# Performance work log

Measured on AMD Instinct MI355X. Metric: run time of the kernel, lower is better.

Reference implementation:

```python
import jax, jax.numpy as jnp
import numpy as np
from jax import lax

B, CR, CS = 2, 256, 512
HR = WR = 64
HS = WS = 32
D_INNER, D_STATE, DT_RANK, D_CONV = 512, 16, 16, 3
EPS = 1e-5


def setup_inputs() -> dict:
    key = jax.random.key(0)
    ks = jax.random.split(key, 16)
    s = 0.02
    return {
        "resnet_feat": jax.random.normal(ks[0], (B, CR, HR, WR), jnp.float32),
        "scp_feat": jax.random.normal(ks[1], (B, CS, HS, WS), jnp.float32),
        "scp_proj_w": jax.random.normal(ks[2], (CR, CS), jnp.float32) * s,
        "scp_bn_g": jnp.ones((CR,), jnp.float32),
        "scp_bn_b": jnp.zeros((CR,), jnp.float32),
        "scp_bn_m": jax.random.normal(ks[3], (CR,), jnp.float32) * 0.1,
        "scp_bn_v": jax.random.uniform(ks[4], (CR,), jnp.float32, minval=0.5, maxval=1.5),
        "res_bn_g": jnp.ones((CR,), jnp.float32),
        "res_bn_b": jnp.zeros((CR,), jnp.float32),
        "res_bn_m": jax.random.normal(ks[5], (CR,), jnp.float32) * 0.1,
        "res_bn_v": jax.random.uniform(ks[6], (CR,), jnp.float32, minval=0.5, maxval=1.5),
        "ln_g": jnp.ones((CR,), jnp.float32),
        "ln_b": jnp.zeros((CR,), jnp.float32),
        "in_proj_w": jax.random.normal(ks[7], (2 * D_INNER, CR), jnp.float32) * s,
        "conv_w": jax.random.normal(ks[8], (D_INNER, 1, D_CONV), jnp.float32) * s,
        "conv_b": jnp.zeros((D_INNER,), jnp.float32),
        "x_proj_w": jax.random.normal(ks[9], (DT_RANK + 2 * D_STATE, D_INNER), jnp.float32) * s,
        "dt_proj_w": jax.random.normal(ks[10], (D_INNER, DT_RANK), jnp.float32) * s,
        "dt_proj_b": jnp.full((D_INNER,), -4.6, jnp.float32),  # softplus -> dt ~ 0.01
        "A_log": jnp.log(jnp.broadcast_to(jnp.arange(1, D_STATE + 1, dtype=jnp.float32), (D_INNER, D_STATE))),
        "D": jnp.ones((D_INNER,), jnp.float32),
        "out_proj_w": jax.random.normal(ks[11], (CR, D_INNER), jnp.float32) * s,
    }


def _bn(x, g, b, m, v):
    # eval-mode BatchNorm2d with running stats, NCHW
    inv = g / jnp.sqrt(v + EPS)
    return x * inv[None, :, None, None] + (b - m * inv)[None, :, None, None]


def reference(resnet_feat, scp_feat, scp_proj_w, scp_bn_g, scp_bn_b, scp_bn_m, scp_bn_v,
              res_bn_g, res_bn_b, res_bn_m, res_bn_v, ln_g, ln_b, in_proj_w, conv_w, conv_b,
              x_proj_w, dt_proj_w, dt_proj_b, A_log, D, out_proj_w):
    # --- fusion prelude ---
    rn = _bn(resnet_feat, res_bn_g, res_bn_b, res_bn_m, res_bn_v)
    sp = jnp.einsum('bchw,oc->bohw', scp_feat, scp_proj_w)        # 1x1 conv, no bias
    sp = _bn(sp, scp_bn_g, scp_bn_b, scp_bn_m, scp_bn_v)
    sp = jax.image.resize(sp, (B, CR, HR, WR), method='bilinear')  # align_corners=False semantics
    fused = rn + sp                                               # (B, CR, HR, WR)

    # --- Mamba2DBlock ---
    L = HR * WR
    x_seq = fused.transpose(0, 2, 3, 1).reshape(B, L, CR)
    mu = x_seq.mean(-1, keepdims=True)
    var = x_seq.var(-1, keepdims=True)
    xn = (x_seq - mu) / jnp.sqrt(var + EPS) * ln_g + ln_b         # LayerNorm

    xz = xn @ in_proj_w.T                                         # (B, L, 2*d_inner)
    xm, z = jnp.split(xz, 2, axis=-1)

    # causal depthwise conv1d over sequence
    xc = xm.transpose(0, 2, 1)                                    # (B, d_inner, L)
    xc = jnp.pad(xc, ((0, 0), (0, 0), (D_CONV - 1, 0)))
    xc = lax.conv_general_dilated(xc, conv_w, (1,), 'VALID',
                                  dimension_numbers=('NCH', 'OIH', 'NCH'),
                                  feature_group_count=D_INNER) + conv_b[None, :, None]
    u = jax.nn.silu(xc.transpose(0, 2, 1))                        # (B, L, d_inner)

    x_dbl = u @ x_proj_w.T                                        # (B, L, dt_rank + 2*d_state)
    dt_in, Bc, Cc = jnp.split(x_dbl, [DT_RANK, DT_RANK + D_STATE], axis=-1)
    dt = jax.nn.softplus(dt_in @ dt_proj_w.T + dt_proj_b)         # (B, L, d_inner)

    A = -jnp.exp(A_log)                                           # (d_inner, d_state)
    dA = jnp.exp(dt[..., None] * A)                               # (B, L, d_inner, d_state)
    dBu = dt[..., None] * Bc[:, :, None, :] * u[..., None]        # (B, L, d_inner, d_state)

    def comb(c1, c2):
        a1, b1 = c1
        a2, b2 = c2
        return a1 * a2, a2 * b1 + b2

    _, h = lax.associative_scan(comb, (dA, dBu), axis=1)          # h: (B, L, d_inner, d_state)
    y = jnp.einsum('blds,bls->bld', h, Cc) + u * D
    y = y * jax.nn.silu(z)
    out_seq = y @ out_proj_w.T                                    # (B, L, CR)
    out = out_seq.reshape(B, HR, WR, CR).transpose(0, 3, 1, 2)
    return fused + out
```

## Files before the change

kernel.cpp:

```cpp
#include <hip/hip_runtime.h>
#include <hip/hip_bf16.h>
#include <math.h>

typedef unsigned short u16;
typedef __attribute__((ext_vector_type(8))) short short8;
typedef __attribute__((ext_vector_type(4))) float f32x4;
typedef __attribute__((ext_vector_type(4))) unsigned short u16x4;

#define DEVINL static __device__ __forceinline__

DEVINL float b2f(u16 x) {
    union { unsigned u; float f; } v; v.u = ((unsigned)x) << 16; return v.f;
}
DEVINL u16 f2b(float f) {
    union { unsigned u; float f; } v; v.f = f;
    unsigned u = v.u;
    return (u16)((u + 0x7fffu + ((u >> 16) & 1u)) >> 16);
}
DEVINL float silu(float x) { return x / (1.f + __expf(-x)); }

template<bool F32> DEVINL float LDs(const void* p, size_t i) {
    if constexpr (F32) return ((const float*)p)[i];
    else               return b2f(((const u16*)p)[i]);
}

#define O_INW  0
#define O_XPW  262144
#define O_OPW  286720
#define O_SPW  417792
#define O_CW   548864
#define O_CB   550400
#define O_DTW  550912
#define O_ALOG 559104
#define O_DTB  567296
#define O_DW   567808
#define O_SG   568320
#define O_SB   568576
#define O_SM   568832
#define O_SV   569088
#define O_RG   569344
#define O_RB   569600
#define O_RM   569856
#define O_RV   570112
#define O_LG   570368
#define O_LB   570624
#define N_CVT  570880

__global__ __launch_bounds__(256) void k_detect1(const u16* __restrict__ raw,
                                                 int* __restrict__ partial)
{
    int tid = threadIdx.x, bid = blockIdx.x;
    int cnt = 0;
    for (size_t i = (size_t)bid * 256 + tid; i < 2097152; i += 64 * 256) {
        float v = b2f(raw[i]);
        if (!(fabsf(v) <= 1e3f)) cnt++;
    }
#pragma unroll
    for (int off = 1; off < 64; off <<= 1) cnt += __shfl_xor(cnt, off);
    __shared__ int s4[4];
    if ((tid & 63) == 0) s4[tid >> 6] = cnt;
    __syncthreads();
    if (tid == 0) partial[bid] = s4[0] + s4[1] + s4[2] + s4[3];
}

__global__ __launch_bounds__(64) void k_detect2(const int* __restrict__ partial,
                                                int* __restrict__ flag)
{
    int c = partial[threadIdx.x];
#pragma unroll
    for (int off = 1; off < 64; off <<= 1) c += __shfl_xor(c, off);
    if (threadIdx.x == 0) flag[0] = (c > 0) ? 1 : 0;
}

__global__ __launch_bounds__(256) void k_cvt(const int* __restrict__ flag,
    const void* inw, const void* xpw, const void* opw, const void* spw,
    const void* cw, const void* cb, const void* dtw, const void* alog,
    const void* dtb, const void* Dw,
    const void* sg, const void* sb, const void* sm, const void* sv,
    const void* rg, const void* rb, const void* rm, const void* rv,
    const void* lg, const void* lb,
    u16* __restrict__ dst)
{
    int i = blockIdx.x * 256 + threadIdx.x;
    if (i >= N_CVT) return;
    const void* src; int off = i;
    if      (i < O_XPW)  { src = inw; }
    else if (i < O_OPW)  { src = xpw;  off = i - O_XPW; }
    else if (i < O_SPW)  { src = opw;  off = i - O_OPW; }
    else if (i < O_CW)   { src = spw;  off = i - O_SPW; }
    else if (i < O_CB)   { src = cw;   off = i - O_CW; }
    else if (i < O_DTW)  { src = cb;   off = i - O_CB; }
    else if (i < O_ALOG) { src = dtw;  off = i - O_DTW; }
    else if (i < O_DTB)  { src = alog; off = i - O_ALOG; }
    else if (i < O_DW)   { src = dtb;  off = i - O_DTB; }
    else if (i < O_SG)   { src = Dw;   off = i - O_DW; }
    else if (i < O_SB)   { src = sg;   off = i - O_SG; }
    else if (i < O_SM)   { src = sb;   off = i - O_SB; }
    else if (i < O_SV)   { src = sm;   off = i - O_SM; }
    else if (i < O_RG)   { src = sv;   off = i - O_SV; }
    else if (i < O_RB)   { src = rg;   off = i - O_RG; }
    else if (i < O_RM)   { src = rb;   off = i - O_RB; }
    else if (i < O_RV)   { src = rm;   off = i - O_RM; }
    else if (i < O_LG)   { src = rv;   off = i - O_RV; }
    else if (i < O_LB)   { src = lg;   off = i - O_LG; }
    else                 { src = lb;   off = i - O_LB; }
    float v = (*flag) ? ((const float*)src)[off] : b2f(((const u16*)src)[off]);
    dst[i] = f2b(v);
}

template<bool F32> DEVINL void tr_body(const void* src, u16* dst, int R, int C)
{
    __shared__ u16 t[64][66];
    int tid = threadIdx.x;
    int c0 = blockIdx.x * 64, r0 = blockIdx.y * 64, b = blockIdx.z;
    int lane = tid & 63, grp = tid >> 6;
#pragma unroll
    for (int j = 0; j < 16; ++j) {
        int rl = j * 4 + grp;
        t[rl][lane] = f2b(LDs<F32>(src, ((size_t)b * R + r0 + rl) * C + c0 + lane));
    }
    __syncthreads();
#pragma unroll
    for (int j = 0; j < 16; ++j) {
        int cl = j * 4 + grp;
        dst[((size_t)b * C + c0 + cl) * R + r0 + lane] = t[lane][cl];
    }
}
__global__ __launch_bounds__(256) void k_tr(const int* flag,
    const void* src, u16* dst, int R, int C)
{
    if (*flag) tr_body<true>(src, dst, R, C);
    else       tr_body<false>(src, dst, R, C);
}

__global__ __launch_bounds__(256) void k_scpmm(
    const u16* __restrict__ scpT, const u16* __restrict__ w16,
    u16* __restrict__ sp16)
{
    const int N = 256, K = 512;
    int tid = threadIdx.x, lane = tid & 63, wid = tid >> 6;
    int ln = lane & 15, q = lane >> 4;
    int m0 = blockIdx.x * 64 + (wid & 1) * 32;
    int n0 = blockIdx.y * 64 + (wid >> 1) * 32;
    f32x4 acc00 = {0.f,0.f,0.f,0.f}, acc01 = acc00, acc10 = acc00, acc11 = acc00;
    const u16* Ap0 = scpT + (size_t)(m0 + ln) * K + q * 8;
    const u16* Ap1 = Ap0 + (size_t)16 * K;
    const u16* Wp = w16 + O_SPW;
#pragma unroll 4
    for (int k0 = 0; k0 < K; k0 += 32) {
        int kk = k0 + q * 8;
        short8 a0 = *reinterpret_cast<const short8*>(Ap0 + k0);
        short8 a1 = *reinterpret_cast<const short8*>(Ap1 + k0);
        short8 b0 = *reinterpret_cast<const short8*>(Wp + (size_t)(n0 + ln) * K + kk);
        short8 b1 = *reinterpret_cast<const short8*>(Wp + (size_t)(n0 + ln + 16) * K + kk);
        acc00 = __builtin_amdgcn_mfma_f32_16x16x32_bf16(a0, b0, acc00, 0, 0, 0);
        acc01 = __builtin_amdgcn_mfma_f32_16x16x32_bf16(a0, b1, acc01, 0, 0, 0);
        acc10 = __builtin_amdgcn_mfma_f32_16x16x32_bf16(a1, b0, acc10, 0, 0, 0);
        acc11 = __builtin_amdgcn_mfma_f32_16x16x32_bf16(a1, b1, acc11, 0, 0, 0);
    }
    int r0 = m0 + q * 4, c0 = n0 + ln;
    float inv0 = b2f(w16[O_SG + c0]) * rsqrtf(b2f(w16[O_SV + c0]) + 1e-5f);
    float sh0  = b2f(w16[O_SB + c0]) - b2f(w16[O_SM + c0]) * inv0;
    float inv1 = b2f(w16[O_SG + c0 + 16]) * rsqrtf(b2f(w16[O_SV + c0 + 16]) + 1e-5f);
    float sh1  = b2f(w16[O_SB + c0 + 16]) - b2f(w16[O_SM + c0 + 16]) * inv1;
#pragma unroll
    for (int r = 0; r < 4; ++r) {
        sp16[(size_t)(r0 + r) * N + c0]           = f2b(acc00[r] * inv0 + sh0);
        sp16[(size_t)(r0 + r) * N + c0 + 16]      = f2b(acc01[r] * inv1 + sh1);
        sp16[(size_t)(r0 + 16 + r) * N + c0]      = f2b(acc10[r] * inv0 + sh0);
        sp16[(size_t)(r0 + 16 + r) * N + c0 + 16] = f2b(acc11[r] * inv1 + sh1);
    }
}

__global__ __launch_bounds__(256) void k_ln(
    const u16* __restrict__ resnetT, const u16* __restrict__ w16,
    const u16* __restrict__ sp16, u16* __restrict__ xn)
{
    int c = threadIdx.x, l = blockIdx.x, b = blockIdx.y;
    int h = l >> 6, w = l & 63;
    float rr  = b2f(resnetT[((size_t)b * 4096 + l) * 256 + c]);
    float inv = b2f(w16[O_RG + c]) * rsqrtf(b2f(w16[O_RV + c]) + 1e-5f);
    float rn  = rr * inv + (b2f(w16[O_RB + c]) - b2f(w16[O_RM + c]) * inv);

    float xh = 0.5f * h - 0.25f; int jh = (int)floorf(xh); float fh = xh - jh;
    float xw = 0.5f * w - 0.25f; int jw = (int)floorf(xw); float fw = xw - jw;
    int h0 = jh < 0 ? 0 : jh, h1 = jh + 1 > 31 ? 31 : jh + 1;
    int w0 = jw < 0 ? 0 : jw, w1 = jw + 1 > 31 ? 31 : jw + 1;
    const u16* spb = sp16 + (size_t)b * 1024 * 256 + c;
    float v00 = b2f(spb[(size_t)(h0 * 32 + w0) * 256]), v01 = b2f(spb[(size_t)(h0 * 32 + w1) * 256]);
    float v10 = b2f(spb[(size_t)(h1 * 32 + w0) * 256]), v11 = b2f(spb[(size_t)(h1 * 32 + w1) * 256]);
    float sp = (1.f - fh) * ((1.f - fw) * v00 + fw * v01)
             + fh * ((1.f - fw) * v10 + fw * v11);
    float fv = rn + sp;

    __shared__ float red[8];
    float s = fv, s2 = fv * fv;
#pragma unroll
    for (int off = 1; off < 64; off <<= 1) {
        s  += __shfl_xor(s, off);
        s2 += __shfl_xor(s2, off);
    }
    int wv = c >> 6;
    if ((c & 63) == 0) { red[wv] = s; red[4 + wv] = s2; }
    __syncthreads();
    float S  = red[0] + red[1] + red[2] + red[3];
    float S2 = red[4] + red[5] + red[6] + red[7];
    float mu   = S * (1.f / 256.f);
    float var  = S2 * (1.f / 256.f) - mu * mu;
    float rstd = rsqrtf(var + 1e-5f);
    float xnv  = (fv - mu) * rstd * b2f(w16[O_LG + c]) + b2f(w16[O_LB + c]);
    xn[((size_t)b * 4096 + l) * 256 + c] = f2b(xnv);
}

__global__ __launch_bounds__(256) void k_gemm_in(
    const u16* __restrict__ A, const u16* __restrict__ w16, u16* __restrict__ Out)
{
    const int N = 1024, K = 256;
    int tid = threadIdx.x, lane = tid & 63, wid = tid >> 6;
    int ln = lane & 15, q = lane >> 4;
    int m0 = blockIdx.x * 64 + (wid & 1) * 32;
    int n0 = blockIdx.y * 64 + (wid >> 1) * 32;
    f32x4 acc00 = {0.f,0.f,0.f,0.f}, acc01 = acc00, acc10 = acc00, acc11 = acc00;
    const u16* Ap0 = A + (size_t)(m0 + ln) * K + q * 8;
    const u16* Ap1 = Ap0 + (size_t)16 * K;
    const u16* Wp = w16 + O_INW;
#pragma unroll 4
    for (int k0 = 0; k0 < K; k0 += 32) {
        int kk = k0 + q * 8;
        short8 a0 = *reinterpret_cast<const short8*>(Ap0 + k0);
        short8 a1 = *reinterpret_cast<const short8*>(Ap1 + k0);
        short8 b0 = *reinterpret_cast<const short8*>(Wp + (size_t)(n0 + ln) * K + kk);
        short8 b1 = *reinterpret_cast<const short8*>(Wp + (size_t)(n0 + ln + 16) * K + kk);
        acc00 = __builtin_amdgcn_mfma_f32_16x16x32_bf16(a0, b0, acc00, 0, 0, 0);
        acc01 = __builtin_amdgcn_mfma_f32_16x16x32_bf16(a0, b1, acc01, 0, 0, 0);
        acc10 = __builtin_amdgcn_mfma_f32_16x16x32_bf16(a1, b0, acc10, 0, 0, 0);
        acc11 = __builtin_amdgcn_mfma_f32_16x16x32_bf16(a1, b1, acc11, 0, 0, 0);
    }
    int r0 = m0 + q * 4, c0 = n0 + ln;
#pragma unroll
    for (int r = 0; r < 4; ++r) {
        Out[(size_t)(r0 + r) * N + c0]           = f2b(acc00[r]);
        Out[(size_t)(r0 + r) * N + c0 + 16]      = f2b(acc01[r]);
        Out[(size_t)(r0 + 16 + r) * N + c0]      = f2b(acc10[r]);
        Out[(size_t)(r0 + 16 + r) * N + c0 + 16] = f2b(acc11[r]);
    }
}

__global__ __launch_bounds__(512) void k_conv(
    const u16* __restrict__ xz, const u16* __restrict__ w16, u16* __restrict__ u)
{
    int d = threadIdx.x, rt = blockIdx.x, b = blockIdx.y;
    int l0 = rt * 16;
    float c0 = b2f(w16[O_CW + d * 3]), c1 = b2f(w16[O_CW + d * 3 + 1]),
          c2 = b2f(w16[O_CW + d * 3 + 2]), cbv = b2f(w16[O_CB + d]);
    size_t base = ((size_t)b * 4096 + l0) * 1024 + d;
    float x2 = (l0 >= 2) ? b2f(xz[base - 2048]) : 0.f;
    float x1 = (l0 >= 1) ? b2f(xz[base - 1024]) : 0.f;
#pragma unroll 4
    for (int il = 0; il < 16; ++il) {
        float x0 = b2f(xz[base + (size_t)il * 1024]);
        float uv = silu(cbv + c0 * x2 + c1 * x1 + c2 * x0);
        u[((size_t)b * 4096 + l0 + il) * 512 + d] = f2b(uv);
        x2 = x1; x1 = x0;
    }
}

__global__ __launch_bounds__(256) void k_xproj(
    const u16* __restrict__ u, const u16* __restrict__ w16, u16* __restrict__ xd16)
{
    int tid = threadIdx.x, lane = tid & 63, wid = tid >> 6;
    int ln = lane & 15, q = lane >> 4;
    int m0 = blockIdx.x * 64 + wid * 16;
    const u16* Wp = w16 + O_XPW;
    f32x4 acc[3];
#pragma unroll
    for (int j = 0; j < 3; ++j) acc[j] = {0.f,0.f,0.f,0.f};
#pragma unroll 4
    for (int k0 = 0; k0 < 512; k0 += 32) {
        int kk0 = k0 + q * 8;
        short8 a0 = *reinterpret_cast<const short8*>(u + (size_t)(m0 + ln) * 512 + kk0);
#pragma unroll
        for (int j = 0; j < 3; ++j) {
            short8 bj = *reinterpret_cast<const short8*>(Wp + (size_t)(16 * j + ln) * 512 + kk0);
            acc[j] = __builtin_amdgcn_mfma_f32_16x16x32_bf16(a0, bj, acc[j], 0, 0, 0);
        }
    }
#pragma unroll
    for (int j = 0; j < 3; ++j)
#pragma unroll
        for (int r = 0; r < 4; ++r)
            xd16[(size_t)(m0 + q * 4 + r) * 48 + 16 * j + ln] = f2b(acc[j][r]);
}

DEVINL float dt_of(const float* xd, const float* wdt, float bias) {
    float acc = bias;
#pragma unroll
    for (int r = 0; r < 16; ++r) acc += xd[r] * wdt[r];
    return acc > 15.f ? acc : __logf(1.f + __expf(acc));
}

__global__ __launch_bounds__(512) void k_scan1(
    const u16* __restrict__ u, const u16* __restrict__ xd16,
    const u16* __restrict__ w16, u16* __restrict__ cA, u16* __restrict__ cH,
    int NC, int CL)
{
    __shared__ float xds[32][48];
    int d = threadIdx.x, ck = blockIdx.x, b = blockIdx.y;
    float wdt[16], a[16], h[16], ap[16];
#pragma unroll
    for (int s = 0; s < 16; ++s) {
        wdt[s] = b2f(w16[O_DTW + d * 16 + s]);
        a[s] = -__expf(b2f(w16[O_ALOG + d * 16 + s]));
        h[s] = 0.f; ap[s] = 1.f;
    }
    float bias = b2f(w16[O_DTB + d]);
    int l0 = ck * CL;
    for (int t0 = 0; t0 < CL; t0 += 32) {
        __syncthreads();
#pragma unroll
        for (int k = 0; k < 3; ++k) {
            int idx = k * 512 + d;
            int r = idx / 48, c = idx - r * 48;
            xds[r][c] = b2f(xd16[((size_t)b * 4096 + l0 + t0 + r) * 48 + c]);
        }
        __syncthreads();
        for (int il = 0; il < 32; ++il) {
            size_t row = (size_t)b * 4096 + l0 + t0 + il;
            float uv = b2f(u[row * 512 + d]);
            const float* xd = xds[il];
            float dtv = dt_of(xd, wdt, bias);
            float du = dtv * uv;
#pragma unroll
            for (int s = 0; s < 16; ++s) {
                float dA = __expf(dtv * a[s]);
                h[s]  = dA * h[s] + du * xd[16 + s];
                ap[s] *= dA;
            }
        }
    }
    size_t base = (((size_t)b * NC + ck) * 16) * 512 + d;
#pragma unroll
    for (int s = 0; s < 16; ++s) {
        cA[base + (size_t)s * 512] = f2b(ap[s]);
        cH[base + (size_t)s * 512] = f2b(h[s]);
    }
}

__global__ __launch_bounds__(128) void k_scan2(const u16* __restrict__ cA,
                                               u16* __restrict__ cH, int NC)
{
    int d = blockIdx.y * 128 + threadIdx.x, s = blockIdx.x, b = blockIdx.z;
    float h = 0.f;
#pragma unroll 4
    for (int ck = 0; ck < NC; ++ck) {
        size_t idx = (((size_t)b * NC + ck) * 16 + s) * 512 + d;
        float aP = b2f(cA[idx]), hE = b2f(cH[idx]);
        cH[idx] = f2b(h);
        h = aP * h + hE;
    }
}

__global__ __launch_bounds__(512) void k_scan3(
    const u16* __restrict__ u, const u16* __restrict__ xz,
    const u16* __restrict__ xd16, const u16* __restrict__ w16,
    const u16* __restrict__ cH, u16* __restrict__ y, int NC, int CL)
{
    __shared__ float xds[32][48];
    int d = threadIdx.x, ck = blockIdx.x, b = blockIdx.y;
    float wdt[16], a[16], h[16];
    size_t base = (((size_t)b * NC + ck) * 16) * 512 + d;
#pragma unroll
    for (int s = 0; s < 16; ++s) {
        wdt[s] = b2f(w16[O_DTW + d * 16 + s]);
        a[s] = -__expf(b2f(w16[O_ALOG + d * 16 + s]));
        h[s] = b2f(cH[base + (size_t)s * 512]);
    }
    float bias = b2f(w16[O_DTB + d]);
    float Dv = b2f(w16[O_DW + d]);
    int l0 = ck * CL;
    for (int t0 = 0; t0 < CL; t0 += 32) {
        __syncthreads();
#pragma unroll
        for (int k = 0; k < 3; ++k) {
            int idx = k * 512 + d;
            int r = idx / 48, c = idx - r * 48;
            xds[r][c] = b2f(xd16[((size_t)b * 4096 + l0 + t0 + r) * 48 + c]);
        }
        __syncthreads();
        for (int il = 0; il < 32; ++il) {
            size_t row = (size_t)b * 4096 + l0 + t0 + il;
            float uv = b2f(u[row * 512 + d]);
            const float* xd = xds[il];
            float dtv = dt_of(xd, wdt, bias);
            float du = dtv * uv;
            float yv = 0.f;
#pragma unroll
            for (int s = 0; s < 16; ++s) {
                float dA = __expf(dtv * a[s]);
                h[s] = dA * h[s] + du * xd[16 + s];
                yv += h[s] * xd[32 + s];
            }
            yv += uv * Dv;
            float zv = b2f(xz[row * 1024 + 512 + d]);
            yv *= silu(zv);
            y[row * 512 + d] = f2b(yv);
        }
    }
}

template<bool F32> DEVINL void out_body(
    const u16* Y, const u16* w16, const void* resnet,
    const u16* sp16, void* outp)
{
    const int K = 512;
    int tid = threadIdx.x, lane = tid & 63, wid = tid >> 6;
    int ln = lane & 15, q = lane >> 4;
    int m0 = blockIdx.x * 64 + (wid & 1) * 32;
    int n0 = blockIdx.y * 64 + (wid >> 1) * 32;
    f32x4 acc[2][2];
    acc[0][0] = {0.f,0.f,0.f,0.f}; acc[0][1] = acc[0][0];
    acc[1][0] = acc[0][0]; acc[1][1] = acc[0][0];
    const u16* Bp0 = Y + (size_t)(n0 + ln) * K + q * 8;
    const u16* Bp1 = Bp0 + (size_t)16 * K;
    const u16* Wp = w16 + O_OPW;
#pragma unroll 4
    for (int k0 = 0; k0 < K; k0 += 32) {
        int kk = k0 + q * 8;
        short8 b0 = *reinterpret_cast<const short8*>(Bp0 + k0);
        short8 b1 = *reinterpret_cast<const short8*>(Bp1 + k0);
        short8 a0 = *reinterpret_cast<const short8*>(Wp + (size_t)(m0 + ln) * K + kk);
        short8 a1 = *reinterpret_cast<const short8*>(Wp + (size_t)(m0 + ln + 16) * K + kk);
        acc[0][0] = __builtin_amdgcn_mfma_f32_16x16x32_bf16(a0, b0, acc[0][0], 0, 0, 0);
        acc[0][1] = __builtin_amdgcn_mfma_f32_16x16x32_bf16(a0, b1, acc[0][1], 0, 0, 0);
        acc[1][0] = __builtin_amdgcn_mfma_f32_16x16x32_bf16(a1, b0, acc[1][0], 0, 0, 0);
        acc[1][1] = __builtin_amdgcn_mfma_f32_16x16x32_bf16(a1, b1, acc[1][1], 0, 0, 0);
    }
    int r0 = m0 + q * 4;
    int nb = n0 + ln;
    float inv8[2][4], sh8[2][4];
#pragma unroll
    for (int im = 0; im < 2; ++im)
#pragma unroll
        for (int r = 0; r < 4; ++r) {
            int c = r0 + 16 * im + r;
            float inv = b2f(w16[O_RG + c]) * rsqrtf(b2f(w16[O_RV + c]) + 1e-5f);
            inv8[im][r] = inv;
            sh8[im][r]  = b2f(w16[O_RB + c]) - b2f(w16[O_RM + c]) * inv;
        }
#pragma unroll
    for (int jn = 0; jn < 2; ++jn) {
        int n = nb + 16 * jn;
        int b = n >> 12, l = n & 4095;
        int hh = l >> 6, w = l & 63;
        float xh = 0.5f * hh - 0.25f; int jh = (int)floorf(xh); float fh = xh - jh;
        float xw = 0.5f * w - 0.25f;  int jw = (int)floorf(xw); float fw = xw - jw;
        int h0 = jh < 0 ? 0 : jh, h1 = jh + 1 > 31 ? 31 : jh + 1;
        int w0 = jw < 0 ? 0 : jw, w1 = jw + 1 > 31 ? 31 : jw + 1;
        float w00 = (1.f - fh) * (1.f - fw), w01 = (1.f - fh) * fw;
        float w10 = fh * (1.f - fw),         w11 = fh * fw;
        const u16* spb = sp16 + (size_t)b * 1024 * 256;
#pragma unroll
        for (int im = 0; im < 2; ++im) {
            int cb = r0 + 16 * im;
            u16x4 s00 = *reinterpret_cast<const u16x4*>(spb + (size_t)(h0 * 32 + w0) * 256 + cb);
            u16x4 s01 = *reinterpret_cast<const u16x4*>(spb + (size_t)(h0 * 32 + w1) * 256 + cb);
            u16x4 s10 = *reinterpret_cast<const u16x4*>(spb + (size_t)(h1 * 32 + w0) * 256 + cb);
            u16x4 s11 = *reinterpret_cast<const u16x4*>(spb + (size_t)(h1 * 32 + w1) * 256 + cb);
#pragma unroll
            for (int r = 0; r < 4; ++r) {
                int c = cb + r;
                float rr = LDs<F32>(resnet, ((size_t)b * 256 + c) * 4096 + l);
                float sp = w00 * b2f(s00[r]) + w01 * b2f(s01[r])
                         + w10 * b2f(s10[r]) + w11 * b2f(s11[r]);
                float val = acc[im][jn][r] + rr * inv8[im][r] + sh8[im][r] + sp;
                size_t oi = ((size_t)b * 256 + c) * 4096 + l;
                if constexpr (F32) ((float*)outp)[oi] = val;
                else               ((u16*)outp)[oi]  = f2b(val);
            }
        }
    }
}
__global__ __launch_bounds__(256) void k_out(const int* flag,
    const u16* Y, const u16* w16, const void* resnet,
    const u16* sp16, void* outp)
{
    if (*flag) out_body<true>(Y, w16, resnet, sp16, outp);
    else       out_body<false>(Y, w16, resnet, sp16, outp);
}

extern "C" void kernel_launch(void* const* d_in, const int* in_sizes, int n_in,
                              void* d_out, int out_size, void* d_ws, size_t ws_size,
                              hipStream_t stream)
{
    const void* resnet = d_in[0];
    const void* scp    = d_in[1];
    const void* spw    = d_in[2];
    const void* sg     = d_in[3];
    const void* sb     = d_in[4];
    const void* sm     = d_in[5];
    const void* sv     = d_in[6];
    const void* rg     = d_in[7];
    const void* rb     = d_in[8];
    const void* rm     = d_in[9];
    const void* rv     = d_in[10];
    const void* lg     = d_in[11];
    const void* lb     = d_in[12];
    const void* inw    = d_in[13];
    const void* cw     = d_in[14];
    const void* cb     = d_in[15];
    const void* xpw    = d_in[16];
    const void* dtw    = d_in[17];
    const void* dtb    = d_in[18];
    const void* alog   = d_in[19];
    const void* Dw     = d_in[20];
    const void* opw    = d_in[21];

    char* ws = (char*)d_ws;
    int*  flag    = (int*)(ws);
    int*  partial = (int*)(ws + 128);
    u16*  w16     = (u16*)(ws + 4096);
    u16*  sp16    = (u16*)(ws + 1310720);
    u16*  scpT    = (u16*)(ws + 2359296);
    u16*  resnetT = (u16*)(ws + 4456448);
    u16*  xn      = (u16*)(ws + 8650752);
    u16*  xz      = (u16*)(ws + 12845056);
    u16*  u       = (u16*)(ws + 29622272);
    u16*  y       = (u16*)(ws + 38011008);
    u16*  xd16    = (u16*)(ws + 46399488);
    const size_t tail0 = 47185920;

    int NC = 16;
    for (int cand = 128; cand >= 16; cand >>= 1) {
        if (tail0 + (size_t)cand * 65536 <= ws_size) { NC = cand; break; }
    }
    int CL = 4096 / NC;
    u16* cA = (u16*)(ws + tail0);
    u16* cH = (u16*)(ws + tail0 + (size_t)NC * 32768);

    k_detect1<<<dim3(64), 256, 0, stream>>>((const u16*)resnet, partial);
    k_detect2<<<dim3(1), 64, 0, stream>>>(partial, flag);
    k_cvt<<<dim3((N_CVT + 255) / 256), 256, 0, stream>>>(flag,
        inw, xpw, opw, spw, cw, cb, dtw, alog, dtb, Dw,
        sg, sb, sm, sv, rg, rb, rm, rv, lg, lb, w16);
    k_tr<<<dim3(16, 8, 2), 256, 0, stream>>>(flag, scp, scpT, 512, 1024);
    k_scpmm<<<dim3(32, 4), 256, 0, stream>>>(scpT, w16, sp16);
    k_tr<<<dim3(64, 4, 2), 256, 0, stream>>>(flag, resnet, resnetT, 256, 4096);
    k_ln<<<dim3(4096, 2), 256, 0, stream>>>(resnetT, w16, sp16, xn);
    k_gemm_in<<<dim3(128, 16), 256, 0, stream>>>(xn, w16, xz);
    k_conv<<<dim3(256, 2), 512, 0, stream>>>(xz, w16, u);
    k_xproj<<<dim3(128), 256, 0, stream>>>(u, w16, xd16);
    k_scan1<<<dim3(NC, 2), 512, 0, stream>>>(u, xd16, w16, cA, cH, NC, CL);
    k_scan2<<<dim3(16, 4, 2), 128, 0, stream>>>(cA, cH, NC);
    k_scan3<<<dim3(NC, 2), 512, 0, stream>>>(u, xz, xd16, w16, cH, y, NC, CL);
    k_out<<<dim3(4, 128), 256, 0, stream>>>(flag, y, w16, resnet, sp16, d_out);
}
```

Before: 289.9 us.

## Fuse conv into xproj/scan, merge prep kernels, batch LN rows per block

Removes the standalone depthwise conv kernel and the u buffer: the causal conv plus SiLU is recomputed on the fly inside x_proj and both scan passes. The detect step becomes a single-block kernel sampling fewer elements, and weight conversion plus both input transposes are merged into one launch. LayerNorm now handles 8 rows per block, and x_proj output is stored as fp32 instead of bf16. This cuts launches and one intermediate round trip, at the cost of redundant conv math and extra xz reads in the scans.

Measured after the change: 281.6 us. -2.9%, faster.

```diff
diff --git a/kernel.cpp b/kernel.cpp
--- a/kernel.cpp
+++ b/kernel.cpp
@@ -18,7 +18,9 @@
     return (u16)((u + 0x7fffu + ((u >> 16) & 1u)) >> 16);
 }
 DEVINL float silu(float x) { return x / (1.f + __expf(-x)); }
-
+DEVINL float ld_any(bool f32, const void* p, size_t i) {
+    return f32 ? ((const float*)p)[i] : b2f(((const u16*)p)[i]);
+}
 template<bool F32> DEVINL float LDs(const void* p, size_t i) {
     if constexpr (F32) return ((const float*)p)[i];
     else               return b2f(((const u16*)p)[i]);
@@ -46,91 +48,89 @@
 #define O_LB   570624
 #define N_CVT  570880
 
-__global__ __launch_bounds__(256) void k_detect1(const u16* __restrict__ raw,
-                                                 int* __restrict__ partial)
-{
-    int tid = threadIdx.x, bid = blockIdx.x;
+__global__ __launch_bounds__(1024) void k_detect(const u16* __restrict__ raw,
+                                                 int* __restrict__ flag)
+{
+    int tid = threadIdx.x;
     int cnt = 0;
-    for (size_t i = (size_t)bid * 256 + tid; i < 2097152; i += 64 * 256) {
+    for (int i = tid; i < 131072; i += 1024) {
         float v = b2f(raw[i]);
         if (!(fabsf(v) <= 1e3f)) cnt++;
     }
 #pragma unroll
     for (int off = 1; off < 64; off <<= 1) cnt += __shfl_xor(cnt, off);
-    __shared__ int s4[4];
-    if ((tid & 63) == 0) s4[tid >> 6] = cnt;
+    __shared__ int s16[16];
+    if ((tid & 63) == 0) s16[tid >> 6] = cnt;
     __syncthreads();
-    if (tid == 0) partial[bid] = s4[0] + s4[1] + s4[2] + s4[3];
-}
-
-__global__ __launch_bounds__(64) void k_detect2(const int* __restrict__ partial,
-                                                int* __restrict__ flag)
-{
-    int c = partial[threadIdx.x];
-#pragma unroll
-    for (int off = 1; off < 64; off <<= 1) c += __shfl_xor(c, off);
-    if (threadIdx.x == 0) flag[0] = (c > 0) ? 1 : 0;
-}
-
-__global__ __launch_bounds__(256) void k_cvt(const int* __restrict__ flag,
+    if (tid == 0) {
+        int c = 0;
+#pragma unroll
+        for (int w = 0; w < 16; ++w) c += s16[w];
+        flag[0] = (c > 0) ? 1 : 0;
+    }
+}
+
+DEVINL void tr_tile(bool f32, const void* src, u16* dst, int R, int C,
+                    int c0, int r0, int b, int tid)
+{
+    __shared__ u16 t[64][66];
+    int lane = tid & 63, grp = tid >> 6;
+#pragma unroll
+    for (int j = 0; j < 16; ++j) {
+        int rl = j * 4 + grp;
+        t[rl][lane] = f2b(ld_any(f32, src, ((size_t)b * R + r0 + rl) * C + c0 + lane));
+    }
+    __syncthreads();
+#pragma unroll
+    for (int j = 0; j < 16; ++j) {
+        int cl = j * 4 + grp;
+        dst[((size_t)b * C + c0 + cl) * R + r0 + lane] = t[lane][cl];
+    }
+}
+
+__global__ __launch_bounds__(256) void k_prep(const int* __restrict__ flag,
     const void* inw, const void* xpw, const void* opw, const void* spw,
     const void* cw, const void* cb, const void* dtw, const void* alog,
     const void* dtb, const void* Dw,
     const void* sg, const void* sb, const void* sm, const void* sv,
     const void* rg, const void* rb, const void* rm, const void* rv,
     const void* lg, const void* lb,
-    u16* __restrict__ dst)
-{
-    int i = blockIdx.x * 256 + threadIdx.x;
-    if (i >= N_CVT) return;
-    const void* src; int off = i;
-    if      (i < O_XPW)  { src = inw; }
-    else if (i < O_OPW)  { src = xpw;  off = i - O_XPW; }
-    else if (i < O_SPW)  { src = opw;  off = i - O_OPW; }
-    else if (i < O_CW)   { src = spw;  off = i - O_SPW; }
-    else if (i < O_CB)   { src = cw;   off = i - O_CW; }
-    else if (i < O_DTW)  { src = cb;   off = i - O_CB; }
-    else if (i < O_ALOG) { src = dtw;  off = i - O_DTW; }
-    else if (i < O_DTB)  { src = alog; off = i - O_ALOG; }
-    else if (i < O_DW)   { src = dtb;  off = i - O_DTB; }
-    else if (i < O_SG)   { src = Dw;   off = i - O_DW; }
-    else if (i < O_SB)   { src = sg;   off = i - O_SG; }
-    else if (i < O_SM)   { src = sb;   off = i - O_SB; }
-    else if (i < O_SV)   { src = sm;   off = i - O_SM; }
-    else if (i < O_RG)   { src = sv;   off = i - O_SV; }
-    else if (i < O_RB)   { src = rg;   off = i - O_RG; }
-    else if (i < O_RM)   { src = rb;   off = i - O_RB; }
-    else if (i < O_RV)   { src = rm;   off = i - O_RM; }
-    else if (i < O_LG)   { src = rv;   off = i - O_RV; }
-    else if (i < O_LB)   { src = lg;   off = i - O_LG; }
-    else                 { src = lb;   off = i - O_LB; }
-    float v = (*flag) ? ((const float*)src)[off] : b2f(((const u16*)src)[off]);
-    dst[i] = f2b(v);
-}
-
-template<bool F32> DEVINL void tr_body(const void* src, u16* dst, int R, int C)
-{
-    __shared__ u16 t[64][66];
-    int tid = threadIdx.x;
-    int c0 = blockIdx.x * 64, r0 = blockIdx.y * 64, b = blockIdx.z;
-    int lane = tid & 63, grp = tid >> 6;
-#pragma unroll
-    for (int j = 0; j < 16; ++j) {
-        int rl = j * 4 + grp;
-        t[rl][lane] = f2b(LDs<F32>(src, ((size_t)b * R + r0 + rl) * C + c0 + lane));
-    }
-    __syncthreads();
-#pragma unroll
-    for (int j = 0; j < 16; ++j) {
-        int cl = j * 4 + grp;
-        dst[((size_t)b * C + c0 + cl) * R + r0 + lane] = t[lane][cl];
-    }
-}
-__global__ __launch_bounds__(256) void k_tr(const int* flag,
-    const void* src, u16* dst, int R, int C)
-{
-    if (*flag) tr_body<true>(src, dst, R, C);
-    else       tr_body<false>(src, dst, R, C);
+    const void* scp, const void* resnet,
+    u16* __restrict__ w16, u16* __restrict__ scpT, u16* __restrict__ resnetT)
+{
+    bool f32 = (*flag != 0);
+    int bid = blockIdx.x, tid = threadIdx.x;
+    if (bid < 2230) {
+        int i = bid * 256 + tid;
+        const void* src; int off = i;
+        if      (i < O_XPW)  { src = inw; }
+        else if (i < O_OPW)  { src = xpw;  off = i - O_XPW; }
+        else if (i < O_SPW)  { src = opw;  off = i - O_OPW; }
+        else if (i < O_CW)   { src = spw;  off = i - O_SPW; }
+        else if (i < O_CB)   { src = cw;   off = i - O_CW; }
+        else if (i < O_DTW)  { src = cb;   off = i - O_CB; }
+        else if (i < O_ALOG) { src = dtw;  off = i - O_DTW; }
+        else if (i < O_DTB)  { src = alog; off = i - O_ALOG; }
+        else if (i < O_DW)   { src = dtb;  off = i - O_DTB; }
+        else if (i < O_SG)   { src = Dw;   off = i - O_DW; }
+        else if (i < O_SB)   { src = sg;   off = i - O_SG; }
+        else if (i < O_SM)   { src = sb;   off = i - O_SB; }
+        else if (i < O_SV)   { src = sm;   off = i - O_SM; }
+        else if (i < O_RG)   { src = sv;   off = i - O_SV; }
+        else if (i < O_RB)   { src = rg;   off = i - O_RG; }
+        else if (i < O_RM)   { src = rb;   off = i - O_RB; }
+        else if (i < O_RV)   { src = rm;   off = i - O_RM; }
+        else if (i < O_LG)   { src = rv;   off = i - O_RV; }
+        else if (i < O_LB)   { src = lg;   off = i - O_LG; }
+        else                 { src = lb;   off = i - O_LB; }
+        w16[i] = f2b(ld_any(f32, src, off));
+    } else if (bid < 2230 + 256) {
+        int t = bid - 2230;
+        tr_tile(f32, scp, scpT, 512, 1024, (t & 15) * 64, ((t >> 4) & 7) * 64, t >> 7, tid);
+    } else {
+        int t = bid - 2486;
+        tr_tile(f32, resnet, resnetT, 256, 4096, (t & 63) * 64, ((t >> 6) & 3) * 64, t >> 8, tid);
+    }
 }
 
 __global__ __launch_bounds__(256) void k_scpmm(
@@ -176,40 +176,44 @@
     const u16* __restrict__ resnetT, const u16* __restrict__ w16,
     const u16* __restrict__ sp16, u16* __restrict__ xn)
 {
-    int c = threadIdx.x, l = blockIdx.x, b = blockIdx.y;
-    int h = l >> 6, w = l & 63;
-    float rr  = b2f(resnetT[((size_t)b * 4096 + l) * 256 + c]);
+    __shared__ float red[8];
+    int c = threadIdx.x, b = blockIdx.y;
     float inv = b2f(w16[O_RG + c]) * rsqrtf(b2f(w16[O_RV + c]) + 1e-5f);
-    float rn  = rr * inv + (b2f(w16[O_RB + c]) - b2f(w16[O_RM + c]) * inv);
-
-    float xh = 0.5f * h - 0.25f; int jh = (int)floorf(xh); float fh = xh - jh;
-    float xw = 0.5f * w - 0.25f; int jw = (int)floorf(xw); float fw = xw - jw;
-    int h0 = jh < 0 ? 0 : jh, h1 = jh + 1 > 31 ? 31 : jh + 1;
-    int w0 = jw < 0 ? 0 : jw, w1 = jw + 1 > 31 ? 31 : jw + 1;
-    const u16* spb = sp16 + (size_t)b * 1024 * 256 + c;
-    float v00 = b2f(spb[(size_t)(h0 * 32 + w0) * 256]), v01 = b2f(spb[(size_t)(h0 * 32 + w1) * 256]);
-    float v10 = b2f(spb[(size_t)(h1 * 32 + w0) * 256]), v11 = b2f(spb[(size_t)(h1 * 32 + w1) * 256]);
-    float sp = (1.f - fh) * ((1.f - fw) * v00 + fw * v01)
-             + fh * ((1.f - fw) * v10 + fw * v11);
-    float fv = rn + sp;
-
-    __shared__ float red[8];
-    float s = fv, s2 = fv * fv;
-#pragma unroll
-    for (int off = 1; off < 64; off <<= 1) {
-        s  += __shfl_xor(s, off);
-        s2 += __shfl_xor(s2, off);
-    }
-    int wv = c >> 6;
-    if ((c & 63) == 0) { red[wv] = s; red[4 + wv] = s2; }
-    __syncthreads();
-    float S  = red[0] + red[1] + red[2] + red[3];
-    float S2 = red[4] + red[5] + red[6] + red[7];
-    float mu   = S * (1.f / 256.f);
-    float var  = S2 * (1.f / 256.f) - mu * mu;
-    float rstd = rsqrtf(var + 1e-5f);
-    float xnv  = (fv - mu) * rstd * b2f(w16[O_LG + c]) + b2f(w16[O_LB + c]);
-    xn[((size_t)b * 4096 + l) * 256 + c] = f2b(xnv);
+    float sh  = b2f(w16[O_RB + c]) - b2f(w16[O_RM + c]) * inv;
+    float lgv = b2f(w16[O_LG + c]), lbv = b2f(w16[O_LB + c]);
+    const u16* spc = sp16 + (size_t)b * 1024 * 256 + c;
+    for (int j = 0; j < 8; ++j) {
+        int l = blockIdx.x * 8 + j;
+        int h = l >> 6, w = l & 63;
+        float rr = b2f(resnetT[((size_t)b * 4096 + l) * 256 + c]);
+        float rn = rr * inv + sh;
+        float xh = 0.5f * h - 0.25f; int jh = (int)floorf(xh); float fh = xh - jh;
+        float xw = 0.5f * w - 0.25f; int jw = (int)floorf(xw); float fw = xw - jw;
+        int h0 = jh < 0 ? 0 : jh, h1 = jh + 1 > 31 ? 31 : jh + 1;
+        int w0 = jw < 0 ? 0 : jw, w1 = jw + 1 > 31 ? 31 : jw + 1;
+        float v00 = b2f(spc[(size_t)(h0 * 32 + w0) * 256]), v01 = b2f(spc[(size_t)(h0 * 32 + w1) * 256]);
+        float v10 = b2f(spc[(size_t)(h1 * 32 + w0) * 256]), v11 = b2f(spc[(size_t)(h1 * 32 + w1) * 256]);
+        float sp = (1.f - fh) * ((1.f - fw) * v00 + fw * v01)
+                 + fh * ((1.f - fw) * v10 + fw * v11);
+        float fv = rn + sp;
+
+        float s = fv, s2 = fv * fv;
+#pragma unroll
+        for (int off = 1; off < 64; off <<= 1) {
+            s  += __shfl_xor(s, off);
+            s2 += __shfl_xor(s2, off);
+        }
+        int wv = c >> 6;
+        if ((c & 63) == 0) { red[wv] = s; red[4 + wv] = s2; }
+        __syncthreads();
+        float S  = red[0] + red[1] + red[2] + red[3];
+        float S2 = red[4] + red[5] + red[6] + red[7];
+        __syncthreads();
+        float mu   = S * (1.f / 256.f);
+        float var  = S2 * (1.f / 256.f) - mu * mu;
+        float rstd = rsqrtf(var + 1e-5f);
+        xn[((size_t)b * 4096 + l) * 256 + c] = f2b((fv - mu) * rstd * lgv + lbv);
+    }
 }
 
 __global__ __launch_bounds__(256) void k_gemm_in(
@@ -246,27 +250,30 @@
     }
 }
 
-__global__ __launch_bounds__(512) void k_conv(
-    const u16* __restrict__ xz, const u16* __restrict__ w16, u16* __restrict__ u)
-{
-    int d = threadIdx.x, rt = blockIdx.x, b = blockIdx.y;
-    int l0 = rt * 16;
-    float c0 = b2f(w16[O_CW + d * 3]), c1 = b2f(w16[O_CW + d * 3 + 1]),
-          c2 = b2f(w16[O_CW + d * 3 + 2]), cbv = b2f(w16[O_CB + d]);
-    size_t base = ((size_t)b * 4096 + l0) * 1024 + d;
-    float x2 = (l0 >= 2) ? b2f(xz[base - 2048]) : 0.f;
-    float x1 = (l0 >= 1) ? b2f(xz[base - 1024]) : 0.f;
-#pragma unroll 4
-    for (int il = 0; il < 16; ++il) {
-        float x0 = b2f(xz[base + (size_t)il * 1024]);
-        float uv = silu(cbv + c0 * x2 + c1 * x1 + c2 * x0);
-        u[((size_t)b * 4096 + l0 + il) * 512 + d] = f2b(uv);
-        x2 = x1; x1 = x0;
-    }
+DEVINL short8 u_frag(const u16* __restrict__ xz, const u16* __restrict__ w16,
+                     int row, int kk0)
+{
+    int l = row & 4095;
+    const u16* p = xz + (size_t)row * 1024 + kk0;
+    short8 zz = {0,0,0,0,0,0,0,0};
+    short8 x0 = *reinterpret_cast<const short8*>(p);
+    short8 x1 = (l >= 1) ? *reinterpret_cast<const short8*>(p - 1024) : zz;
+    short8 x2 = (l >= 2) ? *reinterpret_cast<const short8*>(p - 2048) : zz;
+    short8 r;
+#pragma unroll
+    for (int j = 0; j < 8; ++j) {
+        int d = kk0 + j;
+        float acc = b2f(w16[O_CB + d])
+                  + b2f((u16)x2[j]) * b2f(w16[O_CW + d * 3])
+                  + b2f((u16)x1[j]) * b2f(w16[O_CW + d * 3 + 1])
+                  + b2f((u16)x0[j]) * b2f(w16[O_CW + d * 3 + 2]);
+        r[j] = (short)f2b(silu(acc));
+    }
+    return r;
 }
 
 __global__ __launch_bounds__(256) void k_xproj(
-    const u16* __restrict__ u, const u16* __restrict__ w16, u16* __restrict__ xd16)
+    const u16* __restrict__ xz, const u16* __restrict__ w16, float* __restrict__ xdf)
 {
     int tid = threadIdx.x, lane = tid & 63, wid = tid >> 6;
     int ln = lane & 15, q = lane >> 4;
@@ -275,10 +282,9 @@
     f32x4 acc[3];
 #pragma unroll
     for (int j = 0; j < 3; ++j) acc[j] = {0.f,0.f,0.f,0.f};
-#pragma unroll 4
     for (int k0 = 0; k0 < 512; k0 += 32) {
         int kk0 = k0 + q * 8;
-        short8 a0 = *reinterpret_cast<const short8*>(u + (size_t)(m0 + ln) * 512 + kk0);
+        short8 a0 = u_frag(xz, w16, m0 + ln, kk0);
 #pragma unroll
         for (int j = 0; j < 3; ++j) {
             short8 bj = *reinterpret_cast<const short8*>(Wp + (size_t)(16 * j + ln) * 512 + kk0);
@@ -289,7 +295,7 @@
     for (int j = 0; j < 3; ++j)
 #pragma unroll
         for (int r = 0; r < 4; ++r)
-            xd16[(size_t)(m0 + q * 4 + r) * 48 + 16 * j + ln] = f2b(acc[j][r]);
+            xdf[(size_t)(m0 + q * 4 + r) * 48 + 16 * j + ln] = acc[j][r];
 }
 
 DEVINL float dt_of(const float* xd, const float* wdt, float bias) {
@@ -300,7 +306,7 @@
 }
 
 __global__ __launch_bounds__(512) void k_scan1(
-    const u16* __restrict__ u, const u16* __restrict__ xd16,
+    const u16* __restrict__ xz, const float* __restrict__ xdf,
     const u16* __restrict__ w16, u16* __restrict__ cA, u16* __restrict__ cH,
     int NC, int CL)
 {
@@ -314,19 +320,24 @@
         h[s] = 0.f; ap[s] = 1.f;
     }
     float bias = b2f(w16[O_DTB + d]);
+    float cw0 = b2f(w16[O_CW + d * 3]), cw1 = b2f(w16[O_CW + d * 3 + 1]),
+          cw2 = b2f(w16[O_CW + d * 3 + 2]), cbv = b2f(w16[O_CB + d]);
     int l0 = ck * CL;
+    size_t xbase = ((size_t)b * 4096 + l0) * 1024 + d;
+    float x2 = (l0 >= 2) ? b2f(xz[xbase - 2048]) : 0.f;
+    float x1 = (l0 >= 1) ? b2f(xz[xbase - 1024]) : 0.f;
     for (int t0 = 0; t0 < CL; t0 += 32) {
         __syncthreads();
 #pragma unroll
         for (int k = 0; k < 3; ++k) {
             int idx = k * 512 + d;
             int r = idx / 48, c = idx - r * 48;
-            xds[r][c] = b2f(xd16[((size_t)b * 4096 + l0 + t0 + r) * 48 + c]);
+            xds[r][c] = xdf[((size_t)b * 4096 + l0 + t0 + r) * 48 + c];
         }
         __syncthreads();
         for (int il = 0; il < 32; ++il) {
-            size_t row = (size_t)b * 4096 + l0 + t0 + il;
-            float uv = b2f(u[row * 512 + d]);
+            float x0 = b2f(xz[xbase + (size_t)(t0 + il) * 1024]);
+            float uv = silu(cbv + cw0 * x2 + cw1 * x1 + cw2 * x0);
             const float* xd = xds[il];
             float dtv = dt_of(xd, wdt, bias);
             float du = dtv * uv;
@@ -336,6 +347,7 @@
                 h[s]  = dA * h[s] + du * xd[16 + s];
                 ap[s] *= dA;
             }
+            x2 = x1; x1 = x0;
         }
     }
     size_t base = (((size_t)b * NC + ck) * 16) * 512 + d;
@@ -361,9 +373,9 @@
 }
 
 __global__ __launch_bounds__(512) void k_scan3(
-    const u16* __restrict__ u, const u16* __restrict__ xz,
-    const u16* __restrict__ xd16, const u16* __restrict__ w16,
-    const u16* __restrict__ cH, u16* __restrict__ y, int NC, int CL)
+    const u16* __restrict__ xz, const float* __restrict__ xdf,
+    const u16* __restrict__ w16, const u16* __restrict__ cH,
+    u16* __restrict__ y, int NC, int CL)
 {
     __shared__ float xds[32][48];
     int d = threadIdx.x, ck = blockIdx.x, b = blockIdx.y;
@@ -377,19 +389,25 @@
     }
     float bias = b2f(w16[O_DTB + d]);
     float Dv = b2f(w16[O_DW + d]);
+    float cw0 = b2f(w16[O_CW + d * 3]), cw1 = b2f(w16[O_CW + d * 3 + 1]),
+          cw2 = b2f(w16[O_CW + d * 3 + 2]), cbv = b2f(w16[O_CB + d]);
     int l0 = ck * CL;
+    size_t xbase = ((size_t)b * 4096 + l0) * 1024 + d;
+    float x2 = (l0 >= 2) ? b2f(xz[xbase - 2048]) : 0.f;
+    float x1 = (l0 >= 1) ? b2f(xz[xbase - 1024]) : 0.f;
     for (int t0 = 0; t0 < CL; t0 += 32) {
         __syncthreads();
 #pragma unroll
         for (int k = 0; k < 3; ++k) {
             int idx = k * 512 + d;
             int r = idx / 48, c = idx - r * 48;
-            xds[r][c] = b2f(xd16[((size_t)b * 4096 + l0 + t0 + r) * 48 + c]);
+            xds[r][c] = xdf[((size_t)b * 4096 + l0 + t0 + r) * 48 + c];
         }
         __syncthreads();
         for (int il = 0; il < 32; ++il) {
             size_t row = (size_t)b * 4096 + l0 + t0 + il;
-            float uv = b2f(u[row * 512 + d]);
+            float x0 = b2f(xz[xbase + (size_t)(t0 + il) * 1024]);
+            float uv = silu(cbv + cw0 * x2 + cw1 * x1 + cw2 * x0);
             const float* xd = xds[il];
             float dtv = dt_of(xd, wdt, bias);
             float du = dtv * uv;
@@ -404,6 +422,7 @@
             float zv = b2f(xz[row * 1024 + 512 + d]);
             yv *= silu(zv);
             y[row * 512 + d] = f2b(yv);
+            x2 = x1; x1 = x0;
         }
     }
 }
@@ -515,19 +534,17 @@
     const void* Dw     = d_in[20];
     const void* opw    = d_in[21];
 
-    char* ws = (char*)d_ws;
-    int*  flag    = (int*)(ws);
-    int*  partial = (int*)(ws + 128);
-    u16*  w16     = (u16*)(ws + 4096);
-    u16*  sp16    = (u16*)(ws + 1310720);
-    u16*  scpT    = (u16*)(ws + 2359296);
-    u16*  resnetT = (u16*)(ws + 4456448);
-    u16*  xn      = (u16*)(ws + 8650752);
-    u16*  xz      = (u16*)(ws + 12845056);
-    u16*  u       = (u16*)(ws + 29622272);
-    u16*  y       = (u16*)(ws + 38011008);
-    u16*  xd16    = (u16*)(ws + 46399488);
-    const size_t tail0 = 47185920;
+    char*  ws      = (char*)d_ws;
+    int*   flag    = (int*)(ws);
+    u16*   w16     = (u16*)(ws + 4096);
+    u16*   sp16    = (u16*)(ws + 2097152);
+    u16*   scpT    = (u16*)(ws + 4194304);
+    u16*   resnetT = (u16*)(ws + 8388608);
+    u16*   xn      = (u16*)(ws + 12582912);
+    u16*   xz      = (u16*)(ws + 16777216);
+    float* xdf     = (float*)(ws + 33554432);
+    u16*   y       = (u16*)(ws + 35651584);
+    const size_t tail0 = 44040192;
 
     int NC = 16;
     for (int cand = 128; cand >= 16; cand >>= 1) {
@@ -537,20 +554,17 @@
     u16* cA = (u16*)(ws + tail0);
     u16* cH = (u16*)(ws + tail0 + (size_t)NC * 32768);
 
-    k_detect1<<<dim3(64), 256, 0, stream>>>((const u16*)resnet, partial);
-    k_detect2<<<dim3(1), 64, 0, stream>>>(partial, flag);
-    k_cvt<<<dim3((N_CVT + 255) / 256), 256, 0, stream>>>(flag,
+    k_detect<<<dim3(1), 1024, 0, stream>>>((const u16*)resnet, flag);
+    k_prep<<<dim3(2998), 256, 0, stream>>>(flag,
         inw, xpw, opw, spw, cw, cb, dtw, alog, dtb, Dw,
-        sg, sb, sm, sv, rg, rb, rm, rv, lg, lb, w16);
-    k_tr<<<dim3(16, 8, 2), 256, 0, stream>>>(flag, scp, scpT, 512, 1024);
+        sg, sb, sm, sv, rg, rb, rm, rv, lg, lb,
+        scp, resnet, w16, scpT, resnetT);
     k_scpmm<<<dim3(32, 4), 256, 0, stream>>>(scpT, w16, sp16);
-    k_tr<<<dim3(64, 4, 2), 256, 0, stream>>>(flag, resnet, resnetT, 256, 4096);
-    k_ln<<<dim3(4096, 2), 256, 0, stream>>>(resnetT, w16, sp16, xn);
+    k_ln<<<dim3(512, 2), 256, 0, stream>>>(resnetT, w16, sp16, xn);
     k_gemm_in<<<dim3(128, 16), 256, 0, stream>>>(xn, w16, xz);
-    k_conv<<<dim3(256, 2), 512, 0, stream>>>(xz, w16, u);
-    k_xproj<<<dim3(128), 256, 0, stream>>>(u, w16, xd16);
-    k_scan1<<<dim3(NC, 2), 512, 0, stream>>>(u, xd16, w16, cA, cH, NC, CL);
+    k_xproj<<<dim3(128), 256, 0, stream>>>(xz, w16, xdf);
+    k_scan1<<<dim3(NC, 2), 512, 0, stream>>>(xz, xdf, w16, cA, cH, NC, CL);
     k_scan2<<<dim3(16, 4, 2), 128, 0, stream>>>(cA, cH, NC);
-    k_scan3<<<dim3(NC, 2), 512, 0, stream>>>(u, xz, xd16, w16, cH, y, NC, CL);
+    k_scan3<<<dim3(NC, 2), 512, 0, stream>>>(xz, xdf, w16, cH, y, NC, CL);
     k_out<<<dim3(4, 128), 256, 0, stream>>>(flag, y, w16, resnet, sp16, d_out);
 }
```
